# Kernel optimization log

Measured on AMD Instinct MI355X. Metric: run time of the kernel, lower is better.

Reference implementation:

```python
import jax, jax.numpy as jnp
import numpy as np

BEV_H, BEV_W = 50, 50
D_PILLAR = 4
PC = (-51.2, -51.2, -5.0, 51.2, 51.2, 3.0)
S_IMG = 518.0   # input_size; also img H and W used for uv normalization
LN_EPS = 1e-5
FUSE_EPS = 1e-6
C_CTX = 256


def _layernorm(x):
    mu = jnp.mean(x, axis=-1, keepdims=True)
    var = jnp.mean((x - mu) ** 2, axis=-1, keepdims=True)
    return (x - mu) * jax.lax.rsqrt(var + LN_EPS)


def _make_lidar2img(V):
    # realistic surround-view cameras: yaw-rotated extrinsics + pinhole intrinsics
    fx = fy = 400.0
    cx = cy = S_IMG / 2.0
    K = np.array([[fx, 0, cx, 0], [0, fy, cy, 0], [0, 0, 1, 0], [0, 0, 0, 1]], dtype=np.float64)
    mats = []
    for v in range(V):
        th = 2.0 * np.pi * v / V
        f = np.array([np.cos(th), np.sin(th), 0.0])      # camera forward (z)
        l = np.array([-np.sin(th), np.cos(th), 0.0])     # camera x (lateral)
        d = np.array([0.0, 0.0, -1.0])                   # camera y (down)
        R = np.stack([l, d, f], axis=0)
        t = np.array([0.0, 0.0, 1.5])                    # camera position in lidar frame
        E = np.eye(4); E[:3, :3] = R; E[:3, 3] = -R @ t
        mats.append(K @ E)
    return np.stack(mats, axis=0).astype(np.float32)     # (V,4,4)


def setup_inputs() -> dict:
    key = jax.random.key(0)
    k1, = jax.random.split(key, 1)
    B, V, N, C = 1, 6, 37 * 37, 768
    last_tokens = jax.random.normal(k1, (B, V, N, C), dtype=jnp.float32)
    lidar2img = jnp.asarray(_make_lidar2img(V))[None]    # (B,V,4,4)
    return {
        "last_tokens": last_tokens,
        "lidar2img": lidar2img,
        "w_view": jnp.zeros((1, V, 1), dtype=jnp.float32),
        "post_gamma": jnp.ones((C,), dtype=jnp.float32),
        "post_beta": jnp.zeros((C,), dtype=jnp.float32),
        "logits": jnp.zeros((C_CTX, C // C_CTX), dtype=jnp.float32),
        "patch_h": 37,
        "patch_w": 37,
    }


def _projection(lidar2img, dtype):
    # BEVFormer-style 3d reference points -> per-camera uv + visibility mask
    Z = int(round(PC[5] - PC[2]))  # 8
    zs = (jnp.linspace(0.5, Z - 0.5, D_PILLAR, dtype=dtype) / Z)[:, None, None]
    xs = (jnp.linspace(0.5, BEV_W - 0.5, BEV_W, dtype=dtype) / BEV_W)[None, None, :]
    ys = (jnp.linspace(0.5, BEV_H - 0.5, BEV_H, dtype=dtype) / BEV_H)[None, :, None]
    x, y, z = jnp.broadcast_arrays(xs, ys, zs)           # (D,H,W) each
    ref = jnp.stack([x, y, z], axis=-1).reshape(D_PILLAR, BEV_H * BEV_W, 3)
    ref = ref * jnp.array([PC[3] - PC[0], PC[4] - PC[1], PC[5] - PC[2]], dtype) \
        + jnp.array([PC[0], PC[1], PC[2]], dtype)
    ref4 = jnp.concatenate([ref, jnp.ones_like(ref[..., :1])], axis=-1)  # (D,Q,4)
    pts = jnp.einsum('bvij,dqj->bdvqi', lidar2img, ref4)  # (B,D,V,Q,4)
    zc = pts[..., 2]
    valid = zc > 1e-5
    uv = pts[..., :2] / jnp.maximum(zc, 1e-5)[..., None] / S_IMG
    u, v = uv[..., 0], uv[..., 1]
    valid = valid & (u > 0.0) & (u < 1.0) & (v > 0.0) & (v < 1.0)
    # -> (B,V,Q,D)
    tr = lambda a: jnp.transpose(a, (0, 2, 3, 1))
    return tr(u), tr(v), tr(valid)


def reference(last_tokens, lidar2img, w_view, post_gamma, post_beta, logits, patch_h, patch_w):
    B, V, N, C = last_tokens.shape
    Hp, Wp = int(patch_h), int(patch_w)
    Q = BEV_H * BEV_W
    dt = last_tokens.dtype

    # pre-LN over channels (no affine)
    tok = _layernorm(last_tokens)                         # (B,V,N,C)

    u, v, valid = _projection(lidar2img, dt)              # (B,V,Q,D)
    u, v = jax.lax.stop_gradient(u), jax.lax.stop_gradient(v)  # torch: @no_grad

    # pixel coords on the patch grid (align_corners=True grid_sample equivalent)
    x_p = (u * S_IMG + 0.5) / S_IMG * Wp - 0.5
    y_p = (v * S_IMG + 0.5) / S_IMG * Hp - 0.5

    x0 = jnp.floor(x_p); fx = x_p - x0; x0 = x0.astype(jnp.int32)
    y0 = jnp.floor(y_p); fy = y_p - y0; y0 = y0.astype(jnp.int32)

    QD = Q * D_PILLAR
    acc = jnp.zeros((B, V, QD, C), dtype=dt)
    for dx in (0, 1):
        for dy in (0, 1):
            xi, yi = x0 + dx, y0 + dy
            inb = (xi >= 0) & (xi < Wp) & (yi >= 0) & (yi < Hp)  # zeros padding
            w = jnp.where(dx, fx, 1.0 - fx) * jnp.where(dy, fy, 1.0 - fy) * inb.astype(dt)
            idx = jnp.clip(yi, 0, Hp - 1) * Wp + jnp.clip(xi, 0, Wp - 1)
            g = jnp.take_along_axis(tok, idx.reshape(B, V, QD, 1), axis=2)  # (B,V,QD,C)
            acc = acc + w.reshape(B, V, QD, 1) * g
    sampled = acc.reshape(B, V, Q, D_PILLAR, C)

    m = valid.astype(dt)                                  # (B,V,Q,D)
    feat = jnp.einsum('bvqdc,bvqd->bvqc', sampled, m)     # mask-weighted sum over pillar pts
    cnt = jnp.sum(m, axis=-1)                             # (B,V,Q)

    wv = jax.nn.softplus(w_view)                          # (1,V,1) positive per-view weights
    num = jnp.sum(feat * wv[..., None], axis=1)           # (B,Q,C)
    den = jnp.sum(cnt * wv, axis=1)                       # (B,Q)
    fused = num / (den[..., None] + FUSE_EPS)

    h = _layernorm(fused) * post_gamma + post_beta        # post-LN with affine

    g = C // C_CTX
    wg = jax.nn.softmax(logits, axis=-1)                  # (C_CTX, g)
    y = jnp.sum(h.reshape(B, Q, C_CTX, g) * wg[None, None], axis=-1)  # (B,Q,C_CTX)

    return jnp.transpose(y.reshape(B, BEV_H, BEV_W, C_CTX), (0, 3, 1, 2))
```

## Files before the change

kernel.cpp:

```cpp
#include <hip/hip_runtime.h>
#include <math.h>

#define NV      6
#define ND      4
#define NQ      2500
#define NPATCH  1369
#define CTOK    768
#define HP      37
#define WP      37
#define CCTX    256
#define NGRP    3

__device__ __forceinline__ float softplus_f(float x) {
    return (x > 20.0f) ? x : log1pf(expf(x));
}

__device__ __forceinline__ void block_reduce_2(float& a, float& b, float* sbuf) {
    #pragma unroll
    for (int off = 32; off > 0; off >>= 1) {
        a += __shfl_down(a, off, 64);
        b += __shfl_down(b, off, 64);
    }
    int wave = threadIdx.x >> 6;
    int lane = threadIdx.x & 63;
    if (lane == 0) { sbuf[wave] = a; sbuf[4 + wave] = b; }
    __syncthreads();
    a = sbuf[0] + sbuf[1] + sbuf[2] + sbuf[3];
    b = sbuf[4] + sbuf[5] + sbuf[6] + sbuf[7];
}

__global__ __launch_bounds__(256) void ln_tokens_kernel(
    const float* __restrict__ tok, float* __restrict__ out)
{
    __shared__ float sbuf[8];
    const int t = threadIdx.x;
    const size_t row = blockIdx.x;
    const float* x = tok + row * CTOK;
    float v0 = x[t], v1 = x[t + 256], v2 = x[t + 512];
    float s  = v0 + v1 + v2;
    float ss = v0 * v0 + v1 * v1 + v2 * v2;
    block_reduce_2(s, ss, sbuf);
    float mu  = s * (1.0f / (float)CTOK);
    float var = ss * (1.0f / (float)CTOK) - mu * mu;
    float rs  = rsqrtf(fmaxf(var, 0.0f) + 1e-5f);
    float* o = out + row * CTOK;
    o[t]       = (v0 - mu) * rs;
    o[t + 256] = (v1 - mu) * rs;
    o[t + 512] = (v2 - mu) * rs;
}

__global__ __launch_bounds__(256) void bev_fuse_kernel(
    const float* __restrict__ ln_tok,
    const float* __restrict__ lidar2img,
    const float* __restrict__ w_view,
    const float* __restrict__ gamma,
    const float* __restrict__ beta,
    const float* __restrict__ logits,
    float* __restrict__ out)
{
    __shared__ float s_w[NV * ND * 4];
    __shared__ int   s_idx[NV * ND * 4];
    __shared__ float s_mw[NV * ND];
    __shared__ float sbuf[8];
    __shared__ float s_h[CTOK];

    const int q = blockIdx.x;
    const int t = threadIdx.x;

    if (t < NV * ND) {
        const int v = t >> 2, d = t & 3;
        const int qy = q / 50, qx = q - qy * 50;
        float xf = ((float)qx + 0.5f) * (1.0f / 50.0f);
        float yf = ((float)qy + 0.5f) * (1.0f / 50.0f);
        float zf = (0.5f + (float)d * (7.0f / 3.0f)) * (1.0f / 8.0f);
        float X = xf * 102.4f - 51.2f;
        float Y = yf * 102.4f - 51.2f;
        float Z = zf * 8.0f - 5.0f;
        const float* M = lidar2img + v * 16;
        float px = M[0] * X + M[1] * Y + M[2]  * Z + M[3];
        float py = M[4] * X + M[5] * Y + M[6]  * Z + M[7];
        float pz = M[8] * X + M[9] * Y + M[10] * Z + M[11];
        bool valid = pz > 1e-5f;
        float zc = fmaxf(pz, 1e-5f);
        float uu = px / zc / 518.0f;
        float vv = py / zc / 518.0f;
        valid = valid && (uu > 0.0f) && (uu < 1.0f) && (vv > 0.0f) && (vv < 1.0f);

        if (valid) {
            float wv = softplus_f(w_view[v]);
            s_mw[t] = wv;
            float x_p = (uu * 518.0f + 0.5f) / 518.0f * 37.0f - 0.5f;
            float y_p = (vv * 518.0f + 0.5f) / 518.0f * 37.0f - 0.5f;
            float x0f = floorf(x_p), y0f = floorf(y_p);
            float fx = x_p - x0f, fy = y_p - y0f;
            int x0 = (int)x0f, y0 = (int)y0f;
            #pragma unroll
            for (int corner = 0; corner < 4; ++corner) {
                int dx = corner & 1, dy = corner >> 1;
                int xi = x0 + dx, yi = y0 + dy;
                bool inb = (xi >= 0) && (xi < WP) && (yi >= 0) && (yi < HP);
                float w = (dx ? fx : (1.0f - fx)) * (dy ? fy : (1.0f - fy));
                w = inb ? (w * wv) : 0.0f;
                int xc = min(max(xi, 0), WP - 1);
                int yc = min(max(yi, 0), HP - 1);
                s_w[t * 4 + corner]   = w;
                s_idx[t * 4 + corner] = v * NPATCH + yc * WP + xc;
            }
        } else {
            s_mw[t] = 0.0f;
            #pragma unroll
            for (int corner = 0; corner < 4; ++corner) {
                s_w[t * 4 + corner]   = 0.0f;
                s_idx[t * 4 + corner] = 0;
            }
        }
    }
    __syncthreads();

    float den = 0.0f;
    #pragma unroll
    for (int j = 0; j < NV * ND; ++j) den += s_mw[j];

    float f0 = 0.0f, f1 = 0.0f, f2 = 0.0f;
    for (int j = 0; j < NV * ND * 4; ++j) {
        float w = s_w[j];
        if (w != 0.0f) {
            const float* row = ln_tok + (size_t)s_idx[j] * CTOK;
            f0 = fmaf(w, row[t],       f0);
            f1 = fmaf(w, row[t + 256], f1);
            f2 = fmaf(w, row[t + 512], f2);
        }
    }
    float inv = 1.0f / (den + 1e-6f);
    f0 *= inv; f1 *= inv; f2 *= inv;

    float s  = f0 + f1 + f2;
    float ss = f0 * f0 + f1 * f1 + f2 * f2;
    block_reduce_2(s, ss, sbuf);
    float mu  = s * (1.0f / (float)CTOK);
    float var = ss * (1.0f / (float)CTOK) - mu * mu;
    float rs  = rsqrtf(fmaxf(var, 0.0f) + 1e-5f);

    s_h[t]       = (f0 - mu) * rs * gamma[t]       + beta[t];
    s_h[t + 256] = (f1 - mu) * rs * gamma[t + 256] + beta[t + 256];
    s_h[t + 512] = (f2 - mu) * rs * gamma[t + 512] + beta[t + 512];
    __syncthreads();

    float l0 = logits[t * 3 + 0], l1 = logits[t * 3 + 1], l2 = logits[t * 3 + 2];
    float mx = fmaxf(l0, fmaxf(l1, l2));
    float e0 = expf(l0 - mx), e1 = expf(l1 - mx), e2 = expf(l2 - mx);
    float einv = 1.0f / (e0 + e1 + e2);
    float y = (s_h[t * 3 + 0] * e0 + s_h[t * 3 + 1] * e1 + s_h[t * 3 + 2] * e2) * einv;
    out[(size_t)t * NQ + q] = y;
}

extern "C" void kernel_launch(void* const* d_in, const int* in_sizes, int n_in,
                              void* d_out, int out_size, void* d_ws, size_t ws_size,
                              hipStream_t stream) {
    const float* last_tokens = (const float*)d_in[0];
    const float* lidar2img   = (const float*)d_in[1];
    const float* w_view      = (const float*)d_in[2];
    const float* post_gamma  = (const float*)d_in[3];
    const float* post_beta   = (const float*)d_in[4];
    const float* logits      = (const float*)d_in[5];
    float* out = (float*)d_out;

    float* ln_tok = (float*)d_ws;

    ln_tokens_kernel<<<NV * NPATCH, 256, 0, stream>>>(last_tokens, ln_tok);
    bev_fuse_kernel<<<NQ, 256, 0, stream>>>(ln_tok, lidar2img, w_view,
                                            post_gamma, post_beta, logits, out);
}
```

Measured before the change: 114.7 us.

## Replace normalized token buffer with per-row LN stats folded into bilinear gather

The first kernel now computes only the mean and rstd of each token row, one wave per row, instead of writing a fully normalized copy of all tokens. The fuse kernel gathers raw tokens with float4 loads and folds the normalization algebraically: each gathered row is scaled by weight times rstd, and the weighted sum of means is subtracted afterward. Valid corners are compacted into a shared list with an atomic counter, so zero-weight corners are skipped. This removes a full write and re-read of the roughly 25 MB normalized tensor, at the cost of an order-dependent sum of corners and some idle threads in the gather.

```diff
diff --git a/kernel.cpp b/kernel.cpp
--- a/kernel.cpp
+++ b/kernel.cpp
@@ -5,14 +5,42 @@
 #define ND      4
 #define NQ      2500
 #define NPATCH  1369
+#define NROWS   (NV * NPATCH)
 #define CTOK    768
 #define HP      37
 #define WP      37
 #define CCTX    256
-#define NGRP    3
 
 __device__ __forceinline__ float softplus_f(float x) {
     return (x > 20.0f) ? x : log1pf(expf(x));
+}
+
+__global__ __launch_bounds__(256) void ln_stats_kernel(
+    const float* __restrict__ tok, float* __restrict__ stats )
+{
+    const int wave = threadIdx.x >> 6, lane = threadIdx.x & 63;
+    const int row = blockIdx.x * 4 + wave;
+    if (row >= NROWS) return;
+    const float4* x = (const float4*)(tok + (size_t)row * CTOK);
+    float s = 0.f, ss = 0.f;
+    #pragma unroll
+    for (int i = 0; i < 3; ++i) {
+        float4 v = x[lane + 64 * i];
+        s  += (v.x + v.y) + (v.z + v.w);
+        ss += v.x * v.x + v.y * v.y + v.z * v.z + v.w * v.w;
+    }
+    #pragma unroll
+    for (int off = 32; off; off >>= 1) {
+        s  += __shfl_down(s,  off, 64);
+        ss += __shfl_down(ss, off, 64);
+    }
+    if (lane == 0) {
+        float mu  = s * (1.0f / (float)CTOK);
+        float var = ss * (1.0f / (float)CTOK) - mu * mu;
+        float rs  = rsqrtf(fmaxf(var, 0.0f) + 1e-5f);
+        stats[row * 2 + 0] = mu;
+        stats[row * 2 + 1] = rs;
+    }
 }
 
 __device__ __forceinline__ void block_reduce_2(float& a, float& b, float* sbuf) {
@@ -29,28 +57,9 @@
     b = sbuf[4] + sbuf[5] + sbuf[6] + sbuf[7];
 }
 
-__global__ __launch_bounds__(256) void ln_tokens_kernel(
-    const float* __restrict__ tok, float* __restrict__ out)
-{
-    __shared__ float sbuf[8];
-    const int t = threadIdx.x;
-    const size_t row = blockIdx.x;
-    const float* x = tok + row * CTOK;
-    float v0 = x[t], v1 = x[t + 256], v2 = x[t + 512];
-    float s  = v0 + v1 + v2;
-    float ss = v0 * v0 + v1 * v1 + v2 * v2;
-    block_reduce_2(s, ss, sbuf);
-    float mu  = s * (1.0f / (float)CTOK);
-    float var = ss * (1.0f / (float)CTOK) - mu * mu;
-    float rs  = rsqrtf(fmaxf(var, 0.0f) + 1e-5f);
-    float* o = out + row * CTOK;
-    o[t]       = (v0 - mu) * rs;
-    o[t + 256] = (v1 - mu) * rs;
-    o[t + 512] = (v2 - mu) * rs;
-}
-
 __global__ __launch_bounds__(256) void bev_fuse_kernel(
-    const float* __restrict__ ln_tok,
+    const float* __restrict__ tok,
+    const float* __restrict__ stats,
     const float* __restrict__ lidar2img,
     const float* __restrict__ w_view,
     const float* __restrict__ gamma,
@@ -58,14 +67,19 @@
     const float* __restrict__ logits,
     float* __restrict__ out)
 {
-    __shared__ float s_w[NV * ND * 4];
+    __shared__ float s_b[NV * ND * 4];
+    __shared__ float s_bmu[NV * ND * 4];
     __shared__ int   s_idx[NV * ND * 4];
-    __shared__ float s_mw[NV * ND];
+    __shared__ float s_den[NV * ND];
+    __shared__ int   s_cnt;
     __shared__ float sbuf[8];
     __shared__ float s_h[CTOK];
 
     const int q = blockIdx.x;
     const int t = threadIdx.x;
+
+    if (t == 0) s_cnt = 0;
+    __syncthreads();
 
     if (t < NV * ND) {
         const int v = t >> 2, d = t & 3;
@@ -82,15 +96,16 @@
         float pz = M[8] * X + M[9] * Y + M[10] * Z + M[11];
         bool valid = pz > 1e-5f;
         float zc = fmaxf(pz, 1e-5f);
-        float uu = px / zc / 518.0f;
-        float vv = py / zc / 518.0f;
+        float uu = px / zc * (1.0f / 518.0f);
+        float vv = py / zc * (1.0f / 518.0f);
         valid = valid && (uu > 0.0f) && (uu < 1.0f) && (vv > 0.0f) && (vv < 1.0f);
 
+        float wv = softplus_f(w_view[v]);
+        s_den[t] = valid ? wv : 0.0f;
+
         if (valid) {
-            float wv = softplus_f(w_view[v]);
-            s_mw[t] = wv;
-            float x_p = (uu * 518.0f + 0.5f) / 518.0f * 37.0f - 0.5f;
-            float y_p = (vv * 518.0f + 0.5f) / 518.0f * 37.0f - 0.5f;
+            float x_p = (uu * 518.0f + 0.5f) * (37.0f / 518.0f) - 0.5f;
+            float y_p = (vv * 518.0f + 0.5f) * (37.0f / 518.0f) - 0.5f;
             float x0f = floorf(x_p), y0f = floorf(y_p);
             float fx = x_p - x0f, fy = y_p - y0f;
             int x0 = (int)x0f, y0 = (int)y0f;
@@ -100,50 +115,62 @@
                 int xi = x0 + dx, yi = y0 + dy;
                 bool inb = (xi >= 0) && (xi < WP) && (yi >= 0) && (yi < HP);
                 float w = (dx ? fx : (1.0f - fx)) * (dy ? fy : (1.0f - fy));
-                w = inb ? (w * wv) : 0.0f;
-                int xc = min(max(xi, 0), WP - 1);
-                int yc = min(max(yi, 0), HP - 1);
-                s_w[t * 4 + corner]   = w;
-                s_idx[t * 4 + corner] = v * NPATCH + yc * WP + xc;
-            }
-        } else {
-            s_mw[t] = 0.0f;
-            #pragma unroll
-            for (int corner = 0; corner < 4; ++corner) {
-                s_w[t * 4 + corner]   = 0.0f;
-                s_idx[t * 4 + corner] = 0;
+                if (inb && w != 0.0f) {
+                    int idx = v * NPATCH + yi * WP + xi;
+                    float b = w * wv * stats[idx * 2 + 1];
+                    int slot = atomicAdd(&s_cnt, 1);
+                    s_b[slot]   = b;
+                    s_bmu[slot] = b * stats[idx * 2 + 0];
+                    s_idx[slot] = idx;
+                }
             }
         }
     }
     __syncthreads();
 
+    const int m = s_cnt;
+
     float den = 0.0f;
     #pragma unroll
-    for (int j = 0; j < NV * ND; ++j) den += s_mw[j];
-
-    float f0 = 0.0f, f1 = 0.0f, f2 = 0.0f;
-    for (int j = 0; j < NV * ND * 4; ++j) {
-        float w = s_w[j];
-        if (w != 0.0f) {
-            const float* row = ln_tok + (size_t)s_idx[j] * CTOK;
-            f0 = fmaf(w, row[t],       f0);
-            f1 = fmaf(w, row[t + 256], f1);
-            f2 = fmaf(w, row[t + 512], f2);
+    for (int j = 0; j < NV * ND; ++j) den += s_den[j];
+    float c0 = 0.0f;
+    for (int j = 0; j < m; ++j) c0 += s_bmu[j];
+
+    float f0 = 0.f, f1 = 0.f, f2 = 0.f, f3 = 0.f;
+    if (t < 192) {
+        const float4* base = (const float4*)tok;
+        for (int j = 0; j < m; ++j) {
+            float b = s_b[j];
+            float4 x = base[(size_t)s_idx[j] * (CTOK / 4) + t];
+            f0 = fmaf(b, x.x, f0);
+            f1 = fmaf(b, x.y, f1);
+            f2 = fmaf(b, x.z, f2);
+            f3 = fmaf(b, x.w, f3);
         }
     }
     float inv = 1.0f / (den + 1e-6f);
-    f0 *= inv; f1 *= inv; f2 *= inv;
-
-    float s  = f0 + f1 + f2;
-    float ss = f0 * f0 + f1 * f1 + f2 * f2;
+    f0 = (f0 - c0) * inv;
+    f1 = (f1 - c0) * inv;
+    f2 = (f2 - c0) * inv;
+    f3 = (f3 - c0) * inv;
+
+    float s = 0.f, ss = 0.f;
+    if (t < 192) {
+        s  = (f0 + f1) + (f2 + f3);
+        ss = f0 * f0 + f1 * f1 + f2 * f2 + f3 * f3;
+    }
     block_reduce_2(s, ss, sbuf);
     float mu  = s * (1.0f / (float)CTOK);
     float var = ss * (1.0f / (float)CTOK) - mu * mu;
     float rs  = rsqrtf(fmaxf(var, 0.0f) + 1e-5f);
 
-    s_h[t]       = (f0 - mu) * rs * gamma[t]       + beta[t];
-    s_h[t + 256] = (f1 - mu) * rs * gamma[t + 256] + beta[t + 256];
-    s_h[t + 512] = (f2 - mu) * rs * gamma[t + 512] + beta[t + 512];
+    if (t < 192) {
+        int c = t * 4;
+        s_h[c + 0] = (f0 - mu) * rs * gamma[c + 0] + beta[c + 0];
+        s_h[c + 1] = (f1 - mu) * rs * gamma[c + 1] + beta[c + 1];
+        s_h[c + 2] = (f2 - mu) * rs * gamma[c + 2] + beta[c + 2];
+        s_h[c + 3] = (f3 - mu) * rs * gamma[c + 3] + beta[c + 3];
+    }
     __syncthreads();
 
     float l0 = logits[t * 3 + 0], l1 = logits[t * 3 + 1], l2 = logits[t * 3 + 2];
@@ -165,9 +192,9 @@
     const float* logits      = (const float*)d_in[5];
     float* out = (float*)d_out;
 
-    float* ln_tok = (float*)d_ws;
-
-    ln_tokens_kernel<<<NV * NPATCH, 256, 0, stream>>>(last_tokens, ln_tok);
-    bev_fuse_kernel<<<NQ, 256, 0, stream>>>(ln_tok, lidar2img, w_view,
+    float* stats = (float*)d_ws;
+
+    ln_stats_kernel<<<(NROWS + 3) / 4, 256, 0, stream>>>(last_tokens, stats);
+    bev_fuse_kernel<<<NQ, 256, 0, stream>>>(last_tokens, stats, lidar2img, w_view,
                                             post_gamma, post_beta, logits, out);
 }
```

Measured after the change: 100.3 us. 1.14x faster.
